# Performance work log

Measured on AMD Instinct MI355X. Metric: run time of the kernel, lower is better.

## Reference

```python
import jax, jax.numpy as jnp
import numpy as np

B, N, C = 2, 2048, 1024
H = 16
HD = C // H  # 64


def setup_inputs() -> dict:
    key = jax.random.key(0)
    ks = jax.random.split(key, 6)
    x = jax.random.normal(ks[0], (B, N, C), dtype=jnp.float32)
    # realistic rotary angles
    inv_freq = 1.0 / (10000.0 ** (np.arange(0, HD, 2, dtype=np.float32) / HD))
    t = np.arange(N, dtype=np.float32)
    freqs = np.outer(t, inv_freq)                      # [N, HD/2]
    emb = np.concatenate([freqs, freqs], axis=-1)      # [N, HD]
    cos = jnp.asarray(np.cos(emb), dtype=jnp.float32)
    sin = jnp.asarray(np.sin(emb), dtype=jnp.float32)
    qkv_w = jax.random.normal(ks[1], (3 * C, C), dtype=jnp.float32) * (1.0 / np.sqrt(C))
    proj_w = jax.random.normal(ks[2], (C, C), dtype=jnp.float32) * (1.0 / np.sqrt(C))
    proj_b = jnp.zeros((C,), dtype=jnp.float32)
    return {"x": x, "cos": cos, "sin": sin, "qkv_w": qkv_w, "proj_w": proj_w, "proj_b": proj_b}


def _apply_rope(x, cos, sin):
    # x: [B, H, N, HD]; cos/sin: [N, HD] (broadcast over B, H)
    x1, x2 = jnp.split(x, 2, axis=-1)
    rotated = jnp.concatenate([-x2, x1], axis=-1)
    return x * cos + rotated * sin


def reference(x, cos, sin, qkv_w, proj_w, proj_b):
    b, n, c = x.shape
    scale = (c // H) ** (-0.5)
    qkv = jnp.einsum('bnc,dc->bnd', x, qkv_w)          # [B, N, 3C]
    qkv = qkv.reshape(b, n, 3, H, HD).transpose(2, 0, 3, 1, 4)  # [3, B, H, N, HD]
    q, k, v = qkv[0], qkv[1], qkv[2]
    q = _apply_rope(q, cos, sin)
    k = _apply_rope(k, cos, sin)
    attn = jnp.einsum('bhid,bhjd->bhij', q, k) * scale  # [B, H, N, N]
    attn = jax.nn.softmax(attn, axis=-1)
    out = jnp.einsum('bhij,bhjd->bhid', attn, v)        # [B, H, N, HD]
    out = out.transpose(0, 2, 1, 3).reshape(b, n, c)    # [B, N, C]
    return jnp.einsum('bnc,dc->bnd', out, proj_w) + proj_b
```

## Files before the change

kernel.cpp:

```cpp
#include <hip/hip_runtime.h>
#include <stdint.h>

typedef __bf16 bf16;
typedef bf16 bf16x8 __attribute__((ext_vector_type(8)));
typedef float f32x4 __attribute__((ext_vector_type(4)));
typedef float f32x16 __attribute__((ext_vector_type(16)));
typedef unsigned short u16x8 __attribute__((ext_vector_type(8)));
typedef unsigned short u16x4 __attribute__((ext_vector_type(4)));

__device__ __forceinline__ unsigned short f2bfu(float f) {
    union { bf16 h; unsigned short u; } x;
    x.h = (bf16)f;
    return x.u;
}
__device__ __forceinline__ float bfu2f(unsigned short u) {
    union { unsigned int i; float f; } x;
    x.i = ((unsigned int)u) << 16;
    return x.f;
}
__device__ __forceinline__ unsigned int pack2bf(float a, float b) {
    union { bf16 h[2]; unsigned int u; } x;
    x.h[0] = (bf16)a; x.h[1] = (bf16)b;
    return x.u;
}
__device__ __forceinline__ void pl32_swap(unsigned int &a, unsigned int &b) {
    asm volatile("v_permlane32_swap_b32 %0, %1" : "+v"(a), "+v"(b));
}

__device__ __forceinline__ void gld_lds16(const void* g, void* l) {
    __builtin_amdgcn_global_load_lds(
        (const __attribute__((address_space(1))) unsigned int*)(uintptr_t)g,
        (__attribute__((address_space(3))) unsigned int*)(unsigned int)(uintptr_t)l,
        16, 0, 0);
}

__global__ void cast3_kernel(const float* __restrict__ x,
                             const float* __restrict__ w1,
                             const float* __restrict__ w2,
                             unsigned short* __restrict__ ox,
                             unsigned short* __restrict__ o1,
                             unsigned short* __restrict__ o2) {
    int i = blockIdx.x * blockDim.x + threadIdx.x;
    const float* in; unsigned short* out; int k;
    if (i < 524288)       { in = x;  out = ox; k = i; }
    else if (i < 917504)  { in = w1; out = o1; k = i - 524288; }
    else                  { in = w2; out = o2; k = i - 917504; }
    const f32x4* p = (const f32x4*)(in + (size_t)k * 8);
    f32x4 a = p[0], b = p[1];
    u16x8 o;
    o[0]=f2bfu(a[0]); o[1]=f2bfu(a[1]); o[2]=f2bfu(a[2]); o[3]=f2bfu(a[3]);
    o[4]=f2bfu(b[0]); o[5]=f2bfu(b[1]); o[6]=f2bfu(b[2]); o[7]=f2bfu(b[3]);
    *(u16x8*)(out + (size_t)k * 8) = o;
}

__global__ void rope_kernel(unsigned short* __restrict__ qkv,
                            const float* __restrict__ cosp,
                            const float* __restrict__ sinp) {
    int tid = blockIdx.x * blockDim.x + threadIdx.x;
    int i8  = tid & 3;
    int h   = (tid >> 2) & 15;
    int sel = (tid >> 6) & 1;
    int n   = (tid >> 7) & 2047;
    int b   = tid >> 18;
    size_t base = ((size_t)(b*2048 + n))*3072 + sel*1024 + h*64 + i8*8;
    u16x8 x1 = *(u16x8*)(qkv + base);
    u16x8 x2 = *(u16x8*)(qkv + base + 32);
    const f32x4* cp = (const f32x4*)(cosp + n*64 + i8*8);
    const f32x4* sp = (const f32x4*)(sinp + n*64 + i8*8);
    f32x4 c0 = cp[0], c1 = cp[1], s0 = sp[0], s1 = sp[1];
    float scale = sel ? 1.0f : (0.125f * 1.44269504088896f);
    u16x8 o1, o2;
#pragma unroll
    for (int j = 0; j < 8; j++) {
        float cc = (j < 4) ? c0[j] : c1[j-4];
        float ss = (j < 4) ? s0[j] : s1[j-4];
        float a = bfu2f(x1[j]), d = bfu2f(x2[j]);
        o1[j] = f2bfu((a*cc - d*ss) * scale);
        o2[j] = f2bfu((d*cc + a*ss) * scale);
    }
    *(u16x8*)(qkv + base)      = o1;
    *(u16x8*)(qkv + base + 32) = o2;
}

__global__ __launch_bounds__(512, 2) void gemm_qkv8b(
    const unsigned short* __restrict__ A, const unsigned short* __restrict__ B,
    unsigned short* __restrict__ C, int M, int N, int K)
{
    extern __shared__ char smem[];
    int nwgx = gridDim.x;
    int nwg  = nwgx * gridDim.y;
    int orig = blockIdx.y * nwgx + blockIdx.x;
    int cpx  = nwg >> 3;
    int wg   = (orig & 7) * cpx + (orig >> 3);
    int bx = wg % nwgx, by = wg / nwgx;
    int m0 = by << 8, n0 = bx << 7;
    int t  = threadIdx.x;
    int wv = t >> 6, l = t & 63;
    int fr = l & 15, fq = l >> 4;
    int wm = (wv >> 1) << 6;
    int wn = (wv & 1) << 6;

    auto stage = [&](int kt, int bsel) {
        int k0 = kt << 5;
        char* base = smem + bsel * 24576;
#pragma unroll
        for (int j = 0; j < 2; ++j) {
            int y  = (j << 13) + t * 16;
            int ly = y ^ (((y >> 7) & 3) << 4);
            int row = ly >> 6, colu = (ly & 63) >> 1;
            gld_lds16(A + (size_t)(m0 + row) * K + k0 + colu,
                      base + (j << 13) + (wv << 10));
        }
        {
            int y  = t * 16;
            int ly = y ^ (((y >> 7) & 3) << 4);
            int row = ly >> 6, colu = (ly & 63) >> 1;
            gld_lds16(B + (size_t)(n0 + row) * K + k0 + colu,
                      base + 16384 + (wv << 10));
        }
    };

    f32x4 acc[4][4];
#pragma unroll
    for (int i = 0; i < 4; i++)
#pragma unroll
        for (int j = 0; j < 4; j++) acc[i][j] = f32x4{0.f,0.f,0.f,0.f};

    stage(0, 0);
    stage(1, 1);
    int cb = 0;
    for (int kt = 0; kt < 32; ++kt) {
        if (kt < 31) asm volatile("s_waitcnt vmcnt(3)" ::: "memory");
        else         asm volatile("s_waitcnt vmcnt(0)" ::: "memory");
        __builtin_amdgcn_s_barrier();
        if (kt + 2 < 32) {
            int sb = cb - 1; if (sb < 0) sb = 2;
            stage(kt + 2, sb);
        }
        const char* base = smem + cb * 24576;
        bf16x8 af[4], bfr[4];
#pragma unroll
        for (int m = 0; m < 4; ++m) {
            int row = wm + m*16 + fr;
            af[m] = *(const bf16x8*)(base + row*64 + ((fq ^ ((row >> 1) & 3)) << 4));
        }
#pragma unroll
        for (int n = 0; n < 4; ++n) {
            int row = wn + n*16 + fr;
            bfr[n] = *(const bf16x8*)(base + 16384 + row*64 + ((fq ^ ((row >> 1) & 3)) << 4));
        }
        __builtin_amdgcn_s_setprio(1);
#pragma unroll
        for (int m = 0; m < 4; ++m)
#pragma unroll
            for (int n = 0; n < 4; ++n)
                acc[m][n] = __builtin_amdgcn_mfma_f32_16x16x32_bf16(af[m], bfr[n], acc[m][n], 0, 0, 0);
        __builtin_amdgcn_s_setprio(0);
        cb = (cb == 2) ? 0 : cb + 1;
    }
#pragma unroll
    for (int m = 0; m < 4; ++m)
#pragma unroll
        for (int n = 0; n < 4; ++n)
#pragma unroll
            for (int e = 0; e < 4; ++e) {
                int row = m0 + wm + m*16 + fq*4 + e;
                int col = n0 + wn + n*16 + fr;
                C[(size_t)row * N + col] = f2bfu(acc[m][n][e]);
            }
}

template<int OUT_F32>
__global__ __launch_bounds__(256, 2) void gemm_bt(
    const unsigned short* __restrict__ A, const unsigned short* __restrict__ B,
    void* __restrict__ Cp, const float* __restrict__ bias,
    int M, int N, int K)
{
    __shared__ __align__(16) unsigned short As[2][128*32];
    __shared__ __align__(16) unsigned short Bs[2][128*32];
    int nwg  = gridDim.x * gridDim.y;
    int orig = blockIdx.y * gridDim.x + blockIdx.x;
    int qq = nwg >> 3, rr = nwg & 7;
    int xcd = orig & 7, idx = orig >> 3;
    int wg = (xcd < rr) ? (xcd*(qq+1) + idx) : (rr*(qq+1) + (xcd-rr)*qq + idx);
    int bx = wg % gridDim.x, by = wg / gridDim.x;
    int m0 = by * 128, n0 = bx * 128;
    int t = threadIdx.x;
    int w = t >> 6, l = t & 63;
    int c = l & 15, g = l >> 4;
    int wm = (w >> 1) * 64, wn = (w & 1) * 64;

    auto stage = [&](int kt, int bsel) {
#pragma unroll
        for (int r2 = 0; r2 < 2; ++r2) {
            int xb = w*2048 + r2*1024;
            int x  = xb + l*16;
            int lx = x ^ (((x >> 7) & 3) << 4);
            int row  = lx >> 6;
            int colu = (lx & 63) >> 1;
            int k0 = kt << 5;
            gld_lds16(A + (size_t)(m0+row)*K + k0 + colu, (void*)(As[bsel] + (xb >> 1)));
            gld_lds16(B + (size_t)(n0+row)*K + k0 + colu, (void*)(Bs[bsel] + (xb >> 1)));
        }
    };

    f32x4 acc[4][4];
#pragma unroll
    for (int i = 0; i < 4; i++)
#pragma unroll
        for (int j = 0; j < 4; j++) acc[i][j] = f32x4{0.f,0.f,0.f,0.f};

    int nkt = K >> 5;
    stage(0, 0);
    int cur = 0;
    for (int kt = 0; kt < nkt; ++kt) {
        __syncthreads();
        if (kt + 1 < nkt) stage(kt + 1, cur ^ 1);
        const char* Ab = (const char*)As[cur];
        const char* Bb = (const char*)Bs[cur];
        bf16x8 af[4], bfr[4];
#pragma unroll
        for (int i = 0; i < 4; i++) {
            int rowa = wm + i*16 + c;
            int rowb = wn + i*16 + c;
            af[i]  = *(const bf16x8*)(Ab + rowa*64 + ((g ^ ((rowa >> 1) & 3)) << 4));
            bfr[i] = *(const bf16x8*)(Bb + rowb*64 + ((g ^ ((rowb >> 1) & 3)) << 4));
        }
        __builtin_amdgcn_s_setprio(1);
#pragma unroll
        for (int i = 0; i < 4; i++)
#pragma unroll
            for (int j = 0; j < 4; j++)
                acc[i][j] = __builtin_amdgcn_mfma_f32_16x16x32_bf16(af[i], bfr[j], acc[i][j], 0, 0, 0);
        __builtin_amdgcn_s_setprio(0);
        cur ^= 1;
    }
#pragma unroll
    for (int i = 0; i < 4; i++)
#pragma unroll
        for (int j = 0; j < 4; j++)
#pragma unroll
            for (int e = 0; e < 4; e++) {
                int row = m0 + wm + i*16 + g*4 + e;
                int col = n0 + wn + j*16 + c;
                float v = acc[i][j][e];
                if (bias) v += bias[col];
                if (OUT_F32) ((float*)Cp)[(size_t)row*N + col] = v;
                else ((unsigned short*)Cp)[(size_t)row*N + col] = f2bfu(v);
            }
}

__global__ __launch_bounds__(512, 4) void attn_kernel(
    const unsigned short* __restrict__ qkv, unsigned short* __restrict__ outp)
{
    __shared__ __align__(16) char lds[65536];
    int bh = blockIdx.y;
    int b = bh >> 4, h = bh & 15;
    int q0 = blockIdx.x << 7;
    int t = threadIdx.x;
    int w = t >> 6, l = t & 63;
    int pair = w >> 2, wp = w & 3;
    int tp = t & 255;
    int q = l & 31, hi = l >> 5;
    int qw = q0 + wp*32;
    size_t bh_base = ((size_t)b*2048)*3072 + (size_t)h*64;

    auto kbase = [&](int bsel) -> char* { return lds + (((pair << 1) | bsel) << 13); };
    auto vbase = [&](int bsel) -> char* { return lds + 32768 + (((pair << 1) | bsel) << 13); };

    auto stageK = [&](int kv0, int bsel) {
#pragma unroll
        for (int r2 = 0; r2 < 2; ++r2) {
            int xb = wp*2048 + r2*1024;
            int x  = xb + l*16;
            int row  = x >> 7;
            int scolb = (x & 127) ^ ((row & 7) << 4);
            gld_lds16(qkv + bh_base + 1024 + (size_t)(kv0 + row)*3072 + (scolb >> 1),
                      kbase(bsel) + xb);
        }
    };
    auto loadV = [&](int kv0, u16x8 &v0, u16x8 &v1) {
        int p  = tp >> 3;
        int hb = (tp & 7) << 3;
        const unsigned short* src = qkv + bh_base + 2048 + (size_t)(kv0 + 2*p)*3072 + hb;
        v0 = *(const u16x8*)src;
        v1 = *(const u16x8*)(src + 3072);
    };
    auto writeV = [&](const u16x8 &v0, const u16x8 &v1, int bsel) {
        int p  = tp >> 3;
        int hb = (tp & 7) << 3;
        char* vb = vbase(bsel);
#pragma unroll
        for (int e = 0; e < 8; e++) {
            int hd = hb + e;
            int colb = (4*p) ^ ((((hd) ^ (hd >> 3)) & 7) << 4);
            *(unsigned int*)(vb + hd*128 + colb) =
                (unsigned int)v0[e] | ((unsigned int)v1[e] << 16);
        }
    };

    bf16x8 qf[4];
#pragma unroll
    for (int dc = 0; dc < 4; dc++)
        qf[dc] = *(const bf16x8*)(qkv + bh_base + (size_t)(qw + q)*3072 + dc*16 + hi*8);

    f32x16 oacc[2];
#pragma unroll
    for (int e = 0; e < 16; e++) { oacc[0][e] = 0.f; oacc[1][e] = 0.f; }
    float lsum = 0.f;

    int tile0 = pair << 4;
    u16x8 vc0, vc1, vn0, vn1;
    stageK(tile0 << 6, 0);
    loadV(tile0 << 6, vc0, vc1);
    int cur = 0;

    for (int it = 0; it < 16; ++it) {
        writeV(vc0, vc1, cur);
        __syncthreads();
        if (it < 15) {
            int kv0n = (tile0 + it + 1) << 6;
            stageK(kv0n, cur ^ 1);
            loadV(kv0n, vn0, vn1);
        }
        const char* ksb = kbase(cur);
        const char* vtb = vbase(cur);

#pragma unroll
        for (int sblk = 0; sblk < 2; ++sblk) {
            f32x16 st;
#pragma unroll
            for (int e = 0; e < 16; e++) st[e] = 0.f;
            int krow = sblk*32 + q;
            int ksw = (krow & 7) << 4;
            __builtin_amdgcn_s_setprio(1);
#pragma unroll
            for (int dc = 0; dc < 4; ++dc) {
                bf16x8 kf = *(const bf16x8*)(ksb + krow*128 + ((dc*32 + hi*16) ^ ksw));
                st = __builtin_amdgcn_mfma_f32_32x32x16_bf16(kf, qf[dc], st, 0, 0, 0);
            }
            __builtin_amdgcn_s_setprio(0);
            unsigned int wds[8];
#pragma unroll
            for (int m = 0; m < 8; m++) {
                float p0 = __builtin_amdgcn_exp2f(st[2*m]);
                float p1 = __builtin_amdgcn_exp2f(st[2*m+1]);
                lsum += p0 + p1;
                wds[m] = pack2bf(p0, p1);
            }
#pragma unroll
            for (int half = 0; half < 2; ++half) {
                unsigned int a0 = wds[half*4 + 0], b0 = wds[half*4 + 2];
                unsigned int a1 = wds[half*4 + 1], b1 = wds[half*4 + 3];
                pl32_swap(a0, b0);
                pl32_swap(a1, b1);
                union { unsigned int u[4]; bf16x8 v; } pf;
                pf.u[0] = a0; pf.u[1] = a1; pf.u[2] = b0; pf.u[3] = b1;
                int kc = sblk*2 + half;
                __builtin_amdgcn_s_setprio(1);
#pragma unroll
                for (int hdblk = 0; hdblk < 2; ++hdblk) {
                    int hd = hdblk*32 + q;
                    int vsw = ((hd ^ (hd >> 3)) & 7) << 4;
                    bf16x8 vf = *(const bf16x8*)(vtb + hd*128 + ((kc*32 + hi*16) ^ vsw));
                    oacc[hdblk] = __builtin_amdgcn_mfma_f32_32x32x16_bf16(vf, pf.v, oacc[hdblk], 0, 0, 0);
                }
                __builtin_amdgcn_s_setprio(0);
            }
        }
        vc0 = vn0; vc1 = vn1;
        cur ^= 1;
    }
    float lt = lsum + __shfl_xor(lsum, 32, 64);

    __syncthreads();
    int cbase = ((wp << 6) + l) << 7;
    int swl = (l & 7) << 4;
    if (pair == 1) {
#pragma unroll
        for (int j = 0; j < 8; ++j) {
            int hb = j >> 2, qd = j & 3;
            f32x4 v = f32x4{oacc[hb][qd*4+0], oacc[hb][qd*4+1],
                            oacc[hb][qd*4+2], oacc[hb][qd*4+3]};
            *(f32x4*)(lds + cbase + ((j << 4) ^ swl)) = v;
        }
        ((float*)(lds + 32768))[(wp << 6) + l] = lt;
    }
    __syncthreads();
    if (pair == 0) {
#pragma unroll
        for (int j = 0; j < 8; ++j) {
            int hb = j >> 2, qd = j & 3;
            f32x4 v = *(const f32x4*)(lds + cbase + ((j << 4) ^ swl));
#pragma unroll
            for (int e = 0; e < 4; ++e) oacc[hb][qd*4+e] += v[e];
        }
        lt += ((float*)(lds + 32768))[(wp << 6) + l];
        float rinv = 1.0f / lt;
        size_t orow = (size_t)(b*2048 + qw + q) * 1024 + h*64;
#pragma unroll
        for (int hdblk = 0; hdblk < 2; ++hdblk)
#pragma unroll
            for (int quad = 0; quad < 4; ++quad) {
                u16x4 o4;
#pragma unroll
                for (int j = 0; j < 4; j++)
                    o4[j] = f2bfu(oacc[hdblk][quad*4 + j] * rinv);
                *(u16x4*)(outp + orow + hdblk*32 + quad*8 + hi*4) = o4;
            }
    }
}

extern "C" void kernel_launch(void* const* d_in, const int* in_sizes, int n_in,
                              void* d_out, int out_size, void* d_ws, size_t ws_size,
                              hipStream_t stream) {
    const float* x      = (const float*)d_in[0];
    const float* cosp   = (const float*)d_in[1];
    const float* sinp   = (const float*)d_in[2];
    const float* qkv_w  = (const float*)d_in[3];
    const float* proj_w = (const float*)d_in[4];
    const float* proj_b = (const float*)d_in[5];

    char* ws = (char*)d_ws;
    unsigned short* xb     = (unsigned short*)(ws);
    unsigned short* wqkvb  = (unsigned short*)(ws + (size_t)(8u << 20));
    unsigned short* wprojb = (unsigned short*)(ws + (size_t)(14u << 20));
    unsigned short* qkvb   = (unsigned short*)(ws + (size_t)(16u << 20));
    unsigned short* attno  = xb;

    cast3_kernel<<<4096, 256, 0, stream>>>(x, qkv_w, proj_w, xb, wqkvb, wprojb);

    hipFuncSetAttribute((const void*)gemm_qkv8b,
                        hipFuncAttributeMaxDynamicSharedMemorySize, 73728);
    gemm_qkv8b<<<dim3(24, 16), 512, 73728, stream>>>(xb, wqkvb, qkvb, 4096, 3072, 1024);
    rope_kernel<<<2048, 256, 0, stream>>>(qkvb, cosp, sinp);
    attn_kernel<<<dim3(16, 32), 512, 0, stream>>>(qkvb, attno);
    gemm_bt<1><<<dim3(8, 32), 256, 0, stream>>>(attno, wprojb, d_out, proj_b, 4096, 1024, 1024);
}
```

Before: 123.4 us.

## Rewrite QKV GEMM as 256x256 tile with 8-phase interleaved load pipeline

The QKV projection GEMM tile grows from 256x128 to 256x256, and the K step per iteration grows from 32 to 64 with double-buffered 64KB slots (128KB LDS). Each iteration is split into four phases. In each phase, global-to-LDS loads for later K steps are issued between LDS fragment reads and MFMA bursts, with explicit barriers and waitcnts. The goal is more reuse per loaded byte and better overlap of memory with MFMA work. The cost is fewer workgroups (192 instead of 384 on the GPU), a single workgroup per CU because of the LDS size, and more barriers.

```diff
diff --git a/kernel.cpp b/kernel.cpp
--- a/kernel.cpp
+++ b/kernel.cpp
@@ -82,7 +82,7 @@
     *(u16x8*)(qkv + base + 32) = o2;
 }
 
-__global__ __launch_bounds__(512, 2) void gemm_qkv8b(
+__global__ __launch_bounds__(512, 2) void gemm_8ph(
     const unsigned short* __restrict__ A, const unsigned short* __restrict__ B,
     unsigned short* __restrict__ C, int M, int N, int K)
 {
@@ -93,80 +93,92 @@
     int cpx  = nwg >> 3;
     int wg   = (orig & 7) * cpx + (orig >> 3);
     int bx = wg % nwgx, by = wg / nwgx;
-    int m0 = by << 8, n0 = bx << 7;
+    int m0 = by << 8, n0 = bx << 8;
     int t  = threadIdx.x;
     int wv = t >> 6, l = t & 63;
     int fr = l & 15, fq = l >> 4;
-    int wm = (wv >> 1) << 6;
-    int wn = (wv & 1) << 6;
-
-    auto stage = [&](int kt, int bsel) {
-        int k0 = kt << 5;
-        char* base = smem + bsel * 24576;
+    int wm = (wv >> 2) << 7;
+    int wn = (wv & 3) << 6;
+
+    auto stage = [&](int kt, int idx) {
+        int isB = idx & 1, h = idx >> 1;
+        const unsigned short* src = isB ? B : A;
+        int base0 = isB ? n0 : m0;
+        char* dst = smem + ((kt & 1) << 16) + (isB << 15) + (h << 14);
+        int k0 = (kt << 6) + (h << 5);
 #pragma unroll
         for (int j = 0; j < 2; ++j) {
             int y  = (j << 13) + t * 16;
-            int ly = y ^ (((y >> 7) & 3) << 4);
+            int ly = y ^ (((y >> 9) & 1) << 5);
             int row = ly >> 6, colu = (ly & 63) >> 1;
-            gld_lds16(A + (size_t)(m0 + row) * K + k0 + colu,
-                      base + (j << 13) + (wv << 10));
-        }
-        {
-            int y  = t * 16;
-            int ly = y ^ (((y >> 7) & 3) << 4);
-            int row = ly >> 6, colu = (ly & 63) >> 1;
-            gld_lds16(B + (size_t)(n0 + row) * K + k0 + colu,
-                      base + 16384 + (wv << 10));
+            gld_lds16(src + (size_t)(base0 + row) * K + k0 + colu,
+                      dst + (j << 13) + (wv << 10));
         }
     };
 
-    f32x4 acc[4][4];
-#pragma unroll
-    for (int i = 0; i < 4; i++)
-#pragma unroll
-        for (int j = 0; j < 4; j++) acc[i][j] = f32x4{0.f,0.f,0.f,0.f};
-
-    stage(0, 0);
-    stage(1, 1);
-    int cb = 0;
-    for (int kt = 0; kt < 32; ++kt) {
-        if (kt < 31) asm volatile("s_waitcnt vmcnt(3)" ::: "memory");
-        else         asm volatile("s_waitcnt vmcnt(0)" ::: "memory");
-        __builtin_amdgcn_s_barrier();
-        if (kt + 2 < 32) {
-            int sb = cb - 1; if (sb < 0) sb = 2;
-            stage(kt + 2, sb);
-        }
-        const char* base = smem + cb * 24576;
-        bf16x8 af[4], bfr[4];
-#pragma unroll
-        for (int m = 0; m < 4; ++m) {
-            int row = wm + m*16 + fr;
-            af[m] = *(const bf16x8*)(base + row*64 + ((fq ^ ((row >> 1) & 3)) << 4));
-        }
-#pragma unroll
-        for (int n = 0; n < 4; ++n) {
-            int row = wn + n*16 + fr;
-            bfr[n] = *(const bf16x8*)(base + 16384 + row*64 + ((fq ^ ((row >> 1) & 3)) << 4));
-        }
-        __builtin_amdgcn_s_setprio(1);
-#pragma unroll
-        for (int m = 0; m < 4; ++m)
-#pragma unroll
-            for (int n = 0; n < 4; ++n)
-                acc[m][n] = __builtin_amdgcn_mfma_f32_16x16x32_bf16(af[m], bfr[n], acc[m][n], 0, 0, 0);
-        __builtin_amdgcn_s_setprio(0);
-        cb = (cb == 2) ? 0 : cb + 1;
-    }
-#pragma unroll
-    for (int m = 0; m < 4; ++m)
+    f32x4 acc[8][4];
+#pragma unroll
+    for (int m = 0; m < 8; ++m)
+#pragma unroll
+        for (int n = 0; n < 4; ++n) acc[m][n] = f32x4{0.f,0.f,0.f,0.f};
+
+    stage(0,0); stage(0,1); stage(0,2); stage(0,3);
+    stage(1,0); stage(1,1);
+    asm volatile("s_waitcnt vmcnt(4)" ::: "memory");
+    __builtin_amdgcn_s_barrier();
+
+    for (int kt = 0; kt < 16; ++kt) {
+        int slot = (kt & 1) << 16;
+        bf16x8 bfr[4];
+#pragma unroll
+        for (int q = 0; q < 4; ++q) {
+            int kk = q >> 1, mh = q & 1;
+            if (mh == 0) {
+#pragma unroll
+                for (int n = 0; n < 4; ++n) {
+                    int row = wn + n*16 + fr;
+                    bfr[n] = *(const bf16x8*)(smem + slot + 32768 + (kk << 14)
+                              + row*64 + ((fq*16) ^ ((row & 8) ? 32 : 0)));
+                }
+            }
+            bf16x8 af[4];
+#pragma unroll
+            for (int m = 0; m < 4; ++m) {
+                int row = wm + mh*64 + m*16 + fr;
+                af[m] = *(const bf16x8*)(smem + slot + (kk << 14)
+                          + row*64 + ((fq*16) ^ ((row & 8) ? 32 : 0)));
+            }
+            if (q == 0 && kt + 1 < 16) stage(kt + 1, 2);
+            if (q == 1 && kt + 1 < 16) stage(kt + 1, 3);
+            if (q == 2 && kt + 2 < 16) stage(kt + 2, 0);
+            if (q == 3 && kt + 2 < 16) stage(kt + 2, 1);
+            __builtin_amdgcn_s_barrier();
+            asm volatile("s_waitcnt lgkmcnt(0)" ::: "memory");
+            __builtin_amdgcn_sched_barrier(0);
+            __builtin_amdgcn_s_setprio(1);
+#pragma unroll
+            for (int m = 0; m < 4; ++m)
+#pragma unroll
+                for (int n = 0; n < 4; ++n)
+                    acc[mh*4+m][n] = __builtin_amdgcn_mfma_f32_16x16x32_bf16(
+                        af[m], bfr[n], acc[mh*4+m][n], 0, 0, 0);
+            __builtin_amdgcn_s_setprio(0);
+            if (q == 3 && kt < 15) {
+                if (kt + 1 == 15) asm volatile("s_waitcnt vmcnt(0)" ::: "memory");
+                else              asm volatile("s_waitcnt vmcnt(4)" ::: "memory");
+            }
+            __builtin_amdgcn_s_barrier();
+        }
+    }
+#pragma unroll
+    for (int mb = 0; mb < 8; ++mb)
 #pragma unroll
         for (int n = 0; n < 4; ++n)
 #pragma unroll
             for (int e = 0; e < 4; ++e) {
-                int row = m0 + wm + m*16 + fq*4 + e;
+                int row = m0 + wm + mb*16 + fq*4 + e;
                 int col = n0 + wn + n*16 + fr;
-                C[(size_t)row * N + col] = f2bfu(acc[m][n][e]);
+                C[(size_t)row * N + col] = f2bfu(acc[mb][n][e]);
             }
 }
 
@@ -430,9 +442,9 @@
 
     cast3_kernel<<<4096, 256, 0, stream>>>(x, qkv_w, proj_w, xb, wqkvb, wprojb);
 
-    hipFuncSetAttribute((const void*)gemm_qkv8b,
-                        hipFuncAttributeMaxDynamicSharedMemorySize, 73728);
-    gemm_qkv8b<<<dim3(24, 16), 512, 73728, stream>>>(xb, wqkvb, qkvb, 4096, 3072, 1024);
+    hipFuncSetAttribute((const void*)gemm_8ph,
+                        hipFuncAttributeMaxDynamicSharedMemorySize, 131072);
+    gemm_8ph<<<dim3(12, 16), 512, 131072, stream>>>(xb, wqkvb, qkvb, 4096, 3072, 1024);
     rope_kernel<<<2048, 256, 0, stream>>>(qkvb, cosp, sinp);
     attn_kernel<<<dim3(16, 32), 512, 0, stream>>>(qkvb, attno);
     gemm_bt<1><<<dim3(8, 32), 256, 0, stream>>>(attno, wprojb, d_out, proj_b, 4096, 1024, 1024);
```

Result: no change. 123.6 us (+0.2%).
